# Performance work log

Measured on AMD Instinct MI355X. Metric: run time of the kernel, lower is better.

## Reference

```python
import jax, jax.numpy as jnp
import numpy as np

B = 4096      # batch size per view (init arg bs)
D = 256       # embedding dim
TEMP = 0.5    # init arg temp
EPS = 1e-8    # torch CosineSimilarity eps


def setup_inputs() -> dict:
    key = jax.random.key(0)
    k1, k2 = jax.random.split(key)
    return {
        "emb1": jax.random.normal(k1, (B, D), dtype=jnp.float32),
        "emb2": jax.random.normal(k2, (B, D), dtype=jnp.float32),
    }


def reference(emb1, emb2):
    # z: (2B, D)
    z = jnp.concatenate([emb1, emb2], axis=0)
    n = 2 * B
    # Cosine similarity as normalize + GEMM (same math as broadcast CosineSimilarity):
    # sim[i,j] = (z_i . z_j) / max(||z_i||*||z_j||, eps), then / temp
    norms = jnp.linalg.norm(z, axis=-1)                       # (2B,)
    denom = jnp.maximum(norms[:, None] * norms[None, :], EPS)  # (2B,2B)
    sim = (z @ z.T) / denom / TEMP                             # (2B,2B)

    idx = jnp.arange(n)
    # positives: diag(sim, +B) then diag(sim, -B) == sim[i, (i+B) mod 2B]
    pos = sim[idx, (idx + B) % n]                              # (2B,)

    # logits row i = [pos_i, negatives_i] = all sim[i,:] except the diagonal.
    # cross-entropy with label 0: loss_i = -pos_i + logsumexp(row without diag)
    diag_mask = idx[:, None] == idx[None, :]
    sim_masked = jnp.where(diag_mask, -jnp.inf, sim)
    lse = jax.nn.logsumexp(sim_masked, axis=-1)                # (2B,)

    loss = jnp.sum(lse - pos) / n   # CrossEntropyLoss(reduction='sum') / 2B
    return loss
```

## Files before the change

### kernel.cpp

```cpp
#include <hip/hip_runtime.h>
#include <hip/hip_bf16.h>


constexpr int kN  = 8192;
constexpr int kD  = 256;
constexpr int kBH = 4096;
constexpr int kChunks  = 32;
constexpr int kColsPer = kN / kChunks;
constexpr float kSqrtScale = 1.6986436f;
constexpr float kLn2 = 0.6931471805599453f;

typedef __attribute__((ext_vector_type(8))) short bf16x8;
typedef __attribute__((ext_vector_type(4))) float f32x4;

__device__ __forceinline__ unsigned short f2bf(float f) {
  union { float f; unsigned u; } x;
  x.f = f;
  unsigned u = x.u;
  return (unsigned short)((u + 0x7FFFu + ((u >> 16) & 1u)) >> 16);
}
__device__ __forceinline__ float bf2f(unsigned short h) {
  union { unsigned u; float f; } x;
  x.u = ((unsigned)h) << 16;
  return x.f;
}

__global__ void k_normalize(const float* __restrict__ e1,
                            const float* __restrict__ e2,
                            unsigned short* __restrict__ zn,
                            float* __restrict__ s_sum) {
  if (blockIdx.x < 8) {
    float4 z4 = {0.f, 0.f, 0.f, 0.f};
    *reinterpret_cast<float4*>(s_sum + blockIdx.x * 1024 + threadIdx.x * 4) = z4;
  }
  const int wave = threadIdx.x >> 6;
  const int lane = threadIdx.x & 63;
  const int row  = blockIdx.x * 4 + wave;
  const float* src = (row < kBH) ? (e1 + (size_t)row * kD)
                                 : (e2 + (size_t)(row - kBH) * kD);
  float4 v = *reinterpret_cast<const float4*>(src + lane * 4);
  float ssq = v.x * v.x + v.y * v.y + v.z * v.z + v.w * v.w;
#pragma unroll
  for (int m = 1; m < 64; m <<= 1) ssq += __shfl_xor(ssq, m);
  const float invs = kSqrtScale / sqrtf(ssq);
  ushort4 o;
  o.x = f2bf(v.x * invs);
  o.y = f2bf(v.y * invs);
  o.z = f2bf(v.z * invs);
  o.w = f2bf(v.w * invs);
  const int g  = row >> 4;
  const int rr = row & 15;
  const size_t dst = (size_t)g * 4096 + (lane >> 3) * 512 +
                     ((lane >> 1) & 3) * 128 + rr * 8 + (lane & 1) * 4;
  *reinterpret_cast<ushort4*>(zn + dst) = o;
}

__global__ void k_pos(const unsigned short* __restrict__ zn,
                      float* __restrict__ pos_val,
                      float* __restrict__ dacc) {
  const int wave = threadIdx.x >> 6;
  const int lane = threadIdx.x & 63;
  const int i = blockIdx.x * 4 + wave;
  const int j = i + kBH;
  const int rr = i & 15;
  const size_t off = (size_t)(i >> 4) * 4096 + (lane >> 3) * 512 +
                     ((lane >> 1) & 3) * 128 + rr * 8 + (lane & 1) * 4;
  ushort4 ua = *reinterpret_cast<const ushort4*>(zn + off);
  ushort4 ub = *reinterpret_cast<const ushort4*>(zn + off + (size_t)256 * 4096);
  float dij = 0.f, dii = 0.f, djj = 0.f;
  const unsigned short* pa = &ua.x;
  const unsigned short* pb = &ub.x;
#pragma unroll
  for (int q = 0; q < 4; ++q) {
    const float a = bf2f(pa[q]);
    const float b = bf2f(pb[q]);
    dij += a * b;
    dii += a * a;
    djj += b * b;
  }
#pragma unroll
  for (int m = 1; m < 64; m <<= 1) {
    dij += __shfl_xor(dij, m);
    dii += __shfl_xor(dii, m);
    djj += __shfl_xor(djj, m);
  }
  if (lane == 0) {
    const float p = dij * kLn2;
    pos_val[i] = p;
    pos_val[j] = p;
    dacc[i] = dii;
    dacc[j] = djj;
  }
}

__global__ __launch_bounds__(256, 3)
void k_simlse(const unsigned short* __restrict__ zn,
              float* __restrict__ s_sum) {
  const int bid = blockIdx.x;
  const int rt  = bid >> 5;
  const int ch  = bid & 31;
  const int wave = threadIdx.x >> 6;
  const int lane = threadIdx.x & 63;
  const int l15 = lane & 15;
  const int lhi = lane >> 4;
  const int rowBase = rt * 128 + wave * 32;
  const int colBase = ch * kColsPer;

  bf16x8 a0[8], a1[8];
  {
    const unsigned short* ap = zn + (size_t)(rowBase >> 4) * 4096 + lane * 8;
#pragma unroll
    for (int ks = 0; ks < 8; ++ks) {
      a0[ks] = *reinterpret_cast<const bf16x8*>(ap + ks * 512);
      a1[ks] = *reinterpret_cast<const bf16x8*>(ap + 4096 + ks * 512);
    }
  }

  float sacc[2][4] = {{0.f,0.f,0.f,0.f},{0.f,0.f,0.f,0.f}};

  bf16x8 bA[8], bB[8];
  f32x4 accA0, accA1, accB0, accB1;

  const unsigned short* bRoot = zn + lane * 8;

  auto loadA_ = [&](int tile) {
    const unsigned short* bp = bRoot + (size_t)((colBase >> 4) + tile) * 4096;
#pragma unroll
    for (int ks = 0; ks < 8; ++ks)
      bA[ks] = *reinterpret_cast<const bf16x8*>(bp + ks * 512);
  };
  auto loadB_ = [&](int tile) {
    const unsigned short* bp = bRoot + (size_t)((colBase >> 4) + tile) * 4096;
#pragma unroll
    for (int ks = 0; ks < 8; ++ks)
      bB[ks] = *reinterpret_cast<const bf16x8*>(bp + ks * 512);
  };
  auto mfmaA = [&]() {
    accA0 = {0.f,0.f,0.f,0.f};
    accA1 = {0.f,0.f,0.f,0.f};
#pragma unroll
    for (int ks = 0; ks < 8; ++ks) {
      accA0 = __builtin_amdgcn_mfma_f32_16x16x32_bf16(a0[ks], bA[ks], accA0, 0, 0, 0);
      accA1 = __builtin_amdgcn_mfma_f32_16x16x32_bf16(a1[ks], bA[ks], accA1, 0, 0, 0);
    }
  };
  auto mfmaB = [&]() {
    accB0 = {0.f,0.f,0.f,0.f};
    accB1 = {0.f,0.f,0.f,0.f};
#pragma unroll
    for (int ks = 0; ks < 8; ++ks) {
      accB0 = __builtin_amdgcn_mfma_f32_16x16x32_bf16(a0[ks], bB[ks], accB0, 0, 0, 0);
      accB1 = __builtin_amdgcn_mfma_f32_16x16x32_bf16(a1[ks], bB[ks], accB1, 0, 0, 0);
    }
  };
  auto epiA = [&]() {
#pragma unroll
    for (int j = 0; j < 4; ++j) {
      sacc[0][j] += exp2f(accA0[j]);
      sacc[1][j] += exp2f(accA1[j]);
    }
  };
  auto epiB = [&]() {
#pragma unroll
    for (int j = 0; j < 4; ++j) {
      sacc[0][j] += exp2f(accB0[j]);
      sacc[1][j] += exp2f(accB1[j]);
    }
  };

  loadA_(0);
  loadB_(1);
  mfmaA();
#pragma unroll 1
  for (int t = 1; t <= 13; t += 2) {
    loadA_(t + 1);
    mfmaB();
    epiA();
    loadB_(t + 2);
    mfmaA();
    epiB();
  }
  mfmaB();
  epiA();
  epiB();

#pragma unroll
  for (int s = 0; s < 2; ++s) {
#pragma unroll
    for (int j = 0; j < 4; ++j) {
      float sv = sacc[s][j];
#pragma unroll
      for (int m = 1; m < 16; m <<= 1) sv += __shfl_xor(sv, m);
      if (l15 == 0) {
        const int row = rowBase + s * 16 + lhi * 4 + j;
        atomicAdd(&s_sum[row], sv);
      }
    }
  }
}

__global__ void k_final(const float* __restrict__ s_sum,
                        const float* __restrict__ dacc,
                        const float* __restrict__ pos_val,
                        float* __restrict__ out) {
  __shared__ float red[16];
  float acc = 0.0f;
  for (int r = threadIdx.x; r < kN; r += 1024)
    acc += logf(s_sum[r] - exp2f(dacc[r])) - pos_val[r];
#pragma unroll
  for (int m = 1; m < 64; m <<= 1) acc += __shfl_xor(acc, m);
  const int wave = threadIdx.x >> 6;
  const int lane = threadIdx.x & 63;
  if (lane == 0) red[wave] = acc;
  __syncthreads();
  if (threadIdx.x == 0) {
    float t = 0.0f;
#pragma unroll
    for (int w = 0; w < 16; ++w) t += red[w];
    out[0] = t / (float)kN;
  }
}

extern "C" void kernel_launch(void* const* d_in, const int* in_sizes, int n_in,
                              void* d_out, int out_size, void* d_ws, size_t ws_size,
                              hipStream_t stream) {
  const float* e1 = (const float*)d_in[0];
  const float* e2 = (const float*)d_in[1];
  float* out = (float*)d_out;

  unsigned short* zn = (unsigned short*)d_ws;
  float* s_sum   = (float*)((char*)d_ws + (size_t)kN * kD * 2);
  float* dacc    = s_sum + kN;
  float* pos_val = dacc + kN;

  hipLaunchKernelGGL(k_normalize, dim3(kN / 4), dim3(256), 0, stream,
                     e1, e2, zn, s_sum);
  hipLaunchKernelGGL(k_pos, dim3(kBH / 4), dim3(256), 0, stream,
                     zn, pos_val, dacc);
  hipLaunchKernelGGL(k_simlse, dim3(64 * kChunks), dim3(256), 0, stream,
                     zn, s_sum);
  hipLaunchKernelGGL(k_final, dim3(1), dim3(1024), 0, stream,
                     s_sum, dacc, pos_val, out);
}
```

Baseline: 63.74 us.

## Stage shared B tiles through LDS with async global-to-LDS ring buffer

Previously all four waves of a block each loaded the same 16-column B tile from global memory straight into registers. Now each wave loads one quarter of the tile with global_load_lds into a 4-slot LDS ring buffer, and every wave then reads the full tile from LDS. Barriers and vmcnt waits keep three tiles in flight. This cuts redundant global/L2 traffic by four and frees registers, which allows raising the occupancy hint from 3 to 4 blocks per SM. In exchange it adds two barriers per tile, drops the old register-level MFMA/exp overlap, and issues three wasted wrap-around loads at the end.

```diff
diff --git a/kernel.cpp b/kernel.cpp
--- a/kernel.cpp
+++ b/kernel.cpp
@@ -7,6 +7,7 @@
 constexpr int kBH = 4096;
 constexpr int kChunks  = 32;
 constexpr int kColsPer = kN / kChunks;
+constexpr int kNT = kColsPer / 16;
 constexpr float kSqrtScale = 1.6986436f;
 constexpr float kLn2 = 0.6931471805599453f;
 
@@ -23,6 +24,11 @@
   union { unsigned u; float f; } x;
   x.u = ((unsigned)h) << 16;
   return x.f;
+}
+__device__ __forceinline__ void gload_lds16(const short* g, short* l) {
+  __builtin_amdgcn_global_load_lds(
+      (const __attribute__((address_space(1))) void*)g,
+      (__attribute__((address_space(3))) void*)l, 16, 0, 0);
 }
 
 __global__ void k_normalize(const float* __restrict__ e1,
@@ -93,9 +99,11 @@
   }
 }
 
-__global__ __launch_bounds__(256, 3)
+__global__ __launch_bounds__(256, 4)
 void k_simlse(const unsigned short* __restrict__ zn,
               float* __restrict__ s_sum) {
+  __shared__ __align__(16) short ldsB[4][4096];
+
   const int bid = blockIdx.x;
   const int rt  = bid >> 5;
   const int ch  = bid & 31;
@@ -104,7 +112,7 @@
   const int l15 = lane & 15;
   const int lhi = lane >> 4;
   const int rowBase = rt * 128 + wave * 32;
-  const int colBase = ch * kColsPer;
+  const int grpBase = ch * kNT;
 
   bf16x8 a0[8], a1[8];
   {
@@ -116,73 +124,47 @@
     }
   }
 
+  auto stage = [&](int t) {
+    const short* src = (const short*)zn +
+                       (size_t)(grpBase + (t & (kNT - 1))) * 4096 + wave * 1024;
+    short* dst = &ldsB[t & 3][wave * 1024];
+    gload_lds16(src + lane * 8, dst);
+    gload_lds16(src + 512 + lane * 8, dst + 512);
+  };
+
+  stage(0);
+  stage(1);
+  stage(2);
+  asm volatile("s_waitcnt vmcnt(0)" ::: "memory");
+
   float sacc[2][4] = {{0.f,0.f,0.f,0.f},{0.f,0.f,0.f,0.f}};
 
-  bf16x8 bA[8], bB[8];
-  f32x4 accA0, accA1, accB0, accB1;
-
-  const unsigned short* bRoot = zn + lane * 8;
-
-  auto loadA_ = [&](int tile) {
-    const unsigned short* bp = bRoot + (size_t)((colBase >> 4) + tile) * 4096;
+#pragma unroll 1
+  for (int t = 0; t < kNT; ++t) {
+    __builtin_amdgcn_s_barrier();
+    stage(t + 3);
+    asm volatile("s_waitcnt vmcnt(6)" ::: "memory");
+    __builtin_amdgcn_s_barrier();
+
+    const short* bt = &ldsB[t & 3][0];
+    bf16x8 b[8];
 #pragma unroll
     for (int ks = 0; ks < 8; ++ks)
-      bA[ks] = *reinterpret_cast<const bf16x8*>(bp + ks * 512);
-  };
-  auto loadB_ = [&](int tile) {
-    const unsigned short* bp = bRoot + (size_t)((colBase >> 4) + tile) * 4096;
-#pragma unroll
-    for (int ks = 0; ks < 8; ++ks)
-      bB[ks] = *reinterpret_cast<const bf16x8*>(bp + ks * 512);
-  };
-  auto mfmaA = [&]() {
-    accA0 = {0.f,0.f,0.f,0.f};
-    accA1 = {0.f,0.f,0.f,0.f};
+      b[ks] = *reinterpret_cast<const bf16x8*>(bt + ks * 512 + lane * 8);
+
+    f32x4 acc0 = {0.f,0.f,0.f,0.f};
+    f32x4 acc1 = {0.f,0.f,0.f,0.f};
 #pragma unroll
     for (int ks = 0; ks < 8; ++ks) {
-      accA0 = __builtin_amdgcn_mfma_f32_16x16x32_bf16(a0[ks], bA[ks], accA0, 0, 0, 0);
-      accA1 = __builtin_amdgcn_mfma_f32_16x16x32_bf16(a1[ks], bA[ks], accA1, 0, 0, 0);
-    }
-  };
-  auto mfmaB = [&]() {
-    accB0 = {0.f,0.f,0.f,0.f};
-    accB1 = {0.f,0.f,0.f,0.f};
-#pragma unroll
-    for (int ks = 0; ks < 8; ++ks) {
-      accB0 = __builtin_amdgcn_mfma_f32_16x16x32_bf16(a0[ks], bB[ks], accB0, 0, 0, 0);
-      accB1 = __builtin_amdgcn_mfma_f32_16x16x32_bf16(a1[ks], bB[ks], accB1, 0, 0, 0);
-    }
-  };
-  auto epiA = [&]() {
+      acc0 = __builtin_amdgcn_mfma_f32_16x16x32_bf16(a0[ks], b[ks], acc0, 0, 0, 0);
+      acc1 = __builtin_amdgcn_mfma_f32_16x16x32_bf16(a1[ks], b[ks], acc1, 0, 0, 0);
+    }
 #pragma unroll
     for (int j = 0; j < 4; ++j) {
-      sacc[0][j] += exp2f(accA0[j]);
-      sacc[1][j] += exp2f(accA1[j]);
-    }
-  };
-  auto epiB = [&]() {
-#pragma unroll
-    for (int j = 0; j < 4; ++j) {
-      sacc[0][j] += exp2f(accB0[j]);
-      sacc[1][j] += exp2f(accB1[j]);
-    }
-  };
-
-  loadA_(0);
-  loadB_(1);
-  mfmaA();
-#pragma unroll 1
-  for (int t = 1; t <= 13; t += 2) {
-    loadA_(t + 1);
-    mfmaB();
-    epiA();
-    loadB_(t + 2);
-    mfmaA();
-    epiB();
-  }
-  mfmaB();
-  epiA();
-  epiB();
+      sacc[0][j] += exp2f(acc0[j]);
+      sacc[1][j] += exp2f(acc1[j]);
+    }
+  }
 
 #pragma unroll
   for (int s = 0; s < 2; ++s) {
```

After: 57.80 us. 9.3% less time.
